# Performance work log

Hardware: AMD Instinct MI355X
Metric: run time of the kernel (lower is better)

Reference implementation:

```python
import jax, jax.numpy as jnp
import numpy as np

DIM = 192
HEADS = 6
HEAD_DIM = DIM // HEADS
WS = (7, 7, 7)
SHIFT = (3, 3, 3)
RES = (14, 56, 56)
MLP_HIDDEN = DIM * 4
N = WS[0] * WS[1] * WS[2]  # 343 tokens per window
SCALE = HEAD_DIM ** (-0.5)


def _rel_pos_index():
    coords = np.stack(np.meshgrid(np.arange(WS[0]), np.arange(WS[1]), np.arange(WS[2]), indexing='ij'))
    cf = coords.reshape(3, -1)  # (3, N)
    rel = (cf[:, :, None] - cf[:, None, :]).transpose(1, 2, 0).astype(np.int64)  # (N, N, 3)
    rel[..., 0] += WS[0] - 1
    rel[..., 1] += WS[1] - 1
    rel[..., 2] += WS[2] - 1
    rel[..., 0] *= (2 * WS[1] - 1) * (2 * WS[2] - 1)
    rel[..., 1] *= 2 * WS[2] - 1
    return rel.sum(-1)  # (N, N)


def _attn_mask():
    S, H, W = RES
    img = np.zeros((S, H, W), dtype=np.float32)
    cnt = 0
    for s in (slice(0, -WS[0]), slice(-WS[0], -SHIFT[0]), slice(-SHIFT[0], None)):
        for h in (slice(0, -WS[1]), slice(-WS[1], -SHIFT[1]), slice(-SHIFT[1], None)):
            for w in (slice(0, -WS[2]), slice(-WS[2], -SHIFT[2]), slice(-SHIFT[2], None)):
                img[s, h, w] = cnt
                cnt += 1
    m = img.reshape(S // WS[0], WS[0], H // WS[1], WS[1], W // WS[2], WS[2])
    m = m.transpose(0, 2, 4, 1, 3, 5).reshape(-1, N)  # (nW, N)
    diff = m[:, None, :] - m[:, :, None]
    return np.where(diff != 0, -100.0, 0.0).astype(np.float32)  # (nW, N, N)


REL_IDX = jnp.asarray(_rel_pos_index())
ATTN_MASK = jnp.asarray(_attn_mask())


def _window_partition(x):
    # x: (B, S, H, W, C) -> (B*nW, N, C)
    B, S, H, W, C = x.shape
    x = x.reshape(B, S // WS[0], WS[0], H // WS[1], WS[1], W // WS[2], WS[2], C)
    x = x.transpose(0, 1, 3, 5, 2, 4, 6, 7)
    return x.reshape(-1, N, C)


def _window_reverse(wins, B):
    S, H, W = RES
    C = wins.shape[-1]
    x = wins.reshape(B, S // WS[0], H // WS[1], W // WS[2], WS[0], WS[1], WS[2], C)
    x = x.transpose(0, 1, 4, 2, 5, 3, 6, 7)
    return x.reshape(B, S, H, W, C)


def _layernorm(x, g, b):
    mu = x.mean(-1, keepdims=True)
    var = ((x - mu) ** 2).mean(-1, keepdims=True)
    return (x - mu) * jax.lax.rsqrt(var + 1e-5) * g + b


def setup_inputs() -> dict:
    key = jax.random.key(0)
    ks = jax.random.split(key, 16)
    p = lambda k, shape, s=0.02: (jax.random.normal(k, shape, dtype=jnp.float32) * s)
    return {
        'x': jax.random.normal(ks[0], (1, DIM) + RES, dtype=jnp.float32),
        'norm1_g': jnp.ones((DIM,), jnp.float32),
        'norm1_b': jnp.zeros((DIM,), jnp.float32),
        'qkv_w': p(ks[1], (DIM, 3 * DIM)),
        'qkv_b': jnp.zeros((3 * DIM,), jnp.float32),
        'rpb_table': p(ks[2], ((2 * WS[0] - 1) * (2 * WS[1] - 1) * (2 * WS[2] - 1), HEADS)),
        'proj_w': p(ks[3], (DIM, DIM)),
        'proj_b': jnp.zeros((DIM,), jnp.float32),
        'norm2_g': jnp.ones((DIM,), jnp.float32),
        'norm2_b': jnp.zeros((DIM,), jnp.float32),
        'fc1_w': p(ks[4], (DIM, MLP_HIDDEN)),
        'fc1_b': jnp.zeros((MLP_HIDDEN,), jnp.float32),
        'fc2_w': p(ks[5], (MLP_HIDDEN, DIM)),
        'fc2_b': jnp.zeros((DIM,), jnp.float32),
    }


def reference(x, norm1_g, norm1_b, qkv_w, qkv_b, rpb_table, proj_w, proj_b,
              norm2_g, norm2_b, fc1_w, fc1_b, fc2_w, fc2_b):
    B, C, S, H, W = x.shape
    L = S * H * W
    xt = x.transpose(0, 2, 3, 4, 1).reshape(B, L, C)  # b (s h w) c
    shortcut = xt
    xn = _layernorm(xt, norm1_g, norm1_b).reshape(B, S, H, W, C)
    xs = jnp.roll(xn, (-SHIFT[0], -SHIFT[1], -SHIFT[2]), axis=(1, 2, 3))
    xw = _window_partition(xs)  # (B*nW, N, C)
    B_ = xw.shape[0]
    nW = B_ // B

    qkv = (xw @ qkv_w + qkv_b).reshape(B_, N, 3, HEADS, HEAD_DIM)
    q = qkv[:, :, 0].transpose(0, 2, 1, 3) * SCALE  # (B_, h, N, d)
    k = qkv[:, :, 1].transpose(0, 2, 1, 3)
    v = qkv[:, :, 2].transpose(0, 2, 1, 3)

    attn = jnp.einsum('bhnd,bhmd->bhnm', q, k)
    bias = rpb_table[REL_IDX.reshape(-1)].reshape(N, N, HEADS).transpose(2, 0, 1)  # (h, N, N)
    attn = attn + bias[None]
    attn = attn.reshape(B, nW, HEADS, N, N) + ATTN_MASK[None, :, None]
    attn = jax.nn.softmax(attn.reshape(B_, HEADS, N, N), axis=-1)

    out = jnp.einsum('bhnm,bhmd->bhnd', attn, v).transpose(0, 2, 1, 3).reshape(B_, N, C)
    out = out @ proj_w + proj_b

    xr = _window_reverse(out, B)
    xr = jnp.roll(xr, (SHIFT[0], SHIFT[1], SHIFT[2]), axis=(1, 2, 3)).reshape(B, L, C)
    xt = shortcut + xr

    h = _layernorm(xt, norm2_g, norm2_b)
    h = jax.nn.gelu(h @ fc1_w + fc1_b, approximate=False) @ fc2_w + fc2_b
    xt = xt + h

    return xt.reshape(B, S, H, W, C).transpose(0, 4, 1, 2, 3)  # (B, C, S, H, W)
```

## Files before the change

### kernel.cpp

```cpp
#include <hip/hip_runtime.h>
#include <hip/hip_bf16.h>
#include <math.h>

#define L_TOK 43904
#define NWIN 128
#define NTOK 343
#define NHEAD 6
#define SCALE 0.17677669529663687f
#define LOG2E 1.4426950408889634f
#define NMASK -144.26950408889634f
#define BSTRIDE 352
#define FIXMAX 16.0f

typedef __attribute__((ext_vector_type(8))) short short8;
typedef __attribute__((ext_vector_type(4))) float f32x4;

__device__ __forceinline__ unsigned short f2bf(float x) {
    union { float f; unsigned int u; } v; v.f = x;
    unsigned int r = v.u + 0x7fffu + ((v.u >> 16) & 1u);
    return (unsigned short)(r >> 16);
}
__device__ __forceinline__ unsigned int cvtpk(float a, float b) {
    unsigned int r;
    asm volatile("v_cvt_pk_bf16_f32 %0, %1, %2" : "=v"(r) : "v"(a), "v"(b));
    return r;
}
__device__ __forceinline__ void gload16(const void* g, void* l) {
    __builtin_amdgcn_global_load_lds((const __attribute__((address_space(1))) void*)g,
                                     (__attribute__((address_space(3))) void*)l, 16, 0, 0);
}

__device__ __forceinline__ int winrow(int l) {
    int s = l / 3136;
    int rem = l - s * 3136;
    int h = rem / 56;
    int w = rem - h * 56;
    int ps = s + 11; if (ps >= 14) ps -= 14;
    int ph = h + 53; if (ph >= 56) ph -= 56;
    int pw = w + 53; if (pw >= 56) pw -= 56;
    int wi = ((ps / 7) * 8 + ph / 7) * 8 + pw / 7;
    int tk = ((ps % 7) * 7 + ph % 7) * 7 + pw % 7;
    return wi * NTOK + tk;
}

__global__ __launch_bounds__(256) void prep_kernel(
    const float* __restrict__ qkv_w, const float* __restrict__ qkv_b,
    const float* __restrict__ proj_w, const float* __restrict__ fc1_w,
    const float* __restrict__ fc2_w, const float* __restrict__ table,
    unsigned short* __restrict__ qkvT, unsigned short* __restrict__ projT,
    unsigned short* __restrict__ fc1T, unsigned short* __restrict__ fc2T,
    float* __restrict__ qkvb_s, float* __restrict__ biasC) {
    const float qs = SCALE * LOG2E;
    if (blockIdx.x < 576) {
        int stride = 576 * 256;
        int t0 = blockIdx.x * 256 + threadIdx.x;
        for (int i = t0; i < 576 * 192; i += stride) {
            int n = i / 192, k = i - n * 192;
            float v = qkv_w[k * 576 + n];
            if (n < 192) v *= qs;
            qkvT[i] = f2bf(v);
        }
        for (int i = t0; i < 192 * 192; i += stride) {
            int n = i / 192, k = i - n * 192;
            projT[i] = f2bf(proj_w[k * 192 + n]);
        }
        for (int i = t0; i < 768 * 192; i += stride) {
            int n = i / 192, k = i - n * 192;
            fc1T[i] = f2bf(fc1_w[k * 768 + n]);
        }
        for (int i = t0; i < 192 * 768; i += stride) {
            int n = i / 768, k = i - n * 768;
            fc2T[i] = f2bf(fc2_w[k * 192 + n]);
        }
        for (int i = t0; i < 576; i += stride) {
            float v = qkv_b[i]; if (i < 192) v *= qs;
            qkvb_s[i] = v;
        }
    } else {
        int q = blockIdx.x - 576;
        int qs3 = q / 49, qh = (q / 7) % 7, qw = q % 7;
        for (int k = threadIdx.x; k < BSTRIDE; k += 256) {
            if (k < NTOK) {
                int ks = k / 49, kh = (k / 7) % 7, kw = k % 7;
                int idx = ((qs3 - ks + 6) * 13 + (qh - kh + 6)) * 13 + (qw - kw + 6);
                #pragma unroll
                for (int h = 0; h < NHEAD; ++h)
                    biasC[((size_t)h * NTOK + q) * BSTRIDE + k] = table[idx * 6 + h] * LOG2E - FIXMAX;
            } else {
                #pragma unroll
                for (int h = 0; h < NHEAD; ++h)
                    biasC[((size_t)h * NTOK + q) * BSTRIDE + k] = -30000.f;
            }
        }
    }
}

__global__ __launch_bounds__(256) void ln1_part(const float* __restrict__ x,
                                                const float* __restrict__ g, const float* __restrict__ b,
                                                float* __restrict__ xt, unsigned short* __restrict__ xw) {
    __shared__ float tile[192 * 65];
    __shared__ float red[4][64];
    __shared__ float red2[4][64];
    __shared__ float mu_s[64], rs_s[64];
    int l0 = blockIdx.x * 64;
    int tid = threadIdx.x;
    int j = tid & 63, c4 = tid >> 6;
    for (int cb = 0; cb < 192; cb += 4)
        tile[(cb + c4) * 65 + j] = x[(size_t)(cb + c4) * L_TOK + l0 + j];
    __syncthreads();
    float s = 0.f, ss = 0.f;
    for (int c = c4 * 48; c < c4 * 48 + 48; ++c) {
        float v = tile[c * 65 + j];
        s += v; ss += v * v;
    }
    red[c4][j] = s; red2[c4][j] = ss;
    __syncthreads();
    if (tid < 64) {
        float S = red[0][j] + red[1][j] + red[2][j] + red[3][j];
        float SS = red2[0][j] + red2[1][j] + red2[2][j] + red2[3][j];
        float mu = S * (1.f / 192.f);
        float var = SS * (1.f / 192.f) - mu * mu;
        mu_s[j] = mu;
        rs_s[j] = rsqrtf(var + 1e-5f);
    }
    __syncthreads();
    int wave = tid >> 6, lid = tid & 63;
    for (int t = wave; t < 64; t += 4) {
        int l = l0 + t;
        int r = winrow(l);
        float mu = mu_s[t], rs = rs_s[t];
        #pragma unroll
        for (int q = 0; q < 3; ++q) {
            int c = q * 64 + lid;
            float v = tile[c * 65 + t];
            xt[(size_t)l * 192 + c] = v;
            xw[(size_t)r * 192 + c] = f2bf((v - mu) * rs * g[c] + b[c]);
        }
    }
}

template<int EPI, int OUTMODE>
__global__ __launch_bounds__(256, 3) void gemm_bf16(
    const unsigned short* __restrict__ A, const unsigned short* __restrict__ Bt,
    const float* __restrict__ bias, void* __restrict__ Cout,
    const float* __restrict__ xt, int N, int K) {
    __shared__ unsigned char smem[49152];
    unsigned short* sh = (unsigned short*)smem;
    const int tid = threadIdx.x;
    const int m0 = blockIdx.y * 128;
    const int n0 = blockIdx.x * 64;
    const int lane = tid & 63, wv = tid >> 6;
    const int wm = wv >> 1, wn = wv & 1;
    const int lr = lane & 15, lg = lane >> 4;
    const int KT = K >> 6;

    f32x4 acc[4][2];
    #pragma unroll
    for (int i = 0; i < 4; ++i)
        #pragma unroll
        for (int jj = 0; jj < 2; ++jj)
            acc[i][jj] = (f32x4){0.f, 0.f, 0.f, 0.f};

    #define STAGE(BUF, K0) { \
        unsigned short* dst = sh + (BUF) * 12288; \
        _Pragma("unroll") \
        for (int i_ = 0; i_ < 4; ++i_) { \
            int g_ = (i_ * 4 + wv) * 64 + lane; \
            int row_ = g_ >> 3, gc_ = g_ & 7; \
            gload16(A + (size_t)(m0 + row_) * K + (K0) + ((gc_ ^ (row_ & 7)) << 3), dst + g_ * 8); \
        } \
        _Pragma("unroll") \
        for (int i_ = 0; i_ < 2; ++i_) { \
            int g_ = (i_ * 4 + wv) * 64 + lane; \
            int row_ = g_ >> 3, gc_ = g_ & 7; \
            gload16(Bt + (size_t)(n0 + row_) * K + (K0) + ((gc_ ^ (row_ & 7)) << 3), dst + 8192 + g_ * 8); \
        } }

    STAGE(0, 0);
    __syncthreads();
    for (int kt = 0; kt < KT; ++kt) {
        int buf = kt & 1;
        if (kt + 1 < KT) STAGE(buf ^ 1, (kt + 1) << 6);
        const unsigned short* sA = sh + buf * 12288;
        const unsigned short* sB = sA + 8192;
        #pragma unroll
        for (int kk = 0; kk < 2; ++kk) {
            short8 a[4], b[2];
            #pragma unroll
            for (int i = 0; i < 4; ++i) {
                int row = wm * 64 + i * 16 + lr;
                a[i] = *(const short8*)(sA + row * 64 + (((kk * 4 + lg) ^ (lr & 7)) << 3));
            }
            #pragma unroll
            for (int jj = 0; jj < 2; ++jj) {
                int row = wn * 32 + jj * 16 + lr;
                b[jj] = *(const short8*)(sB + row * 64 + (((kk * 4 + lg) ^ (lr & 7)) << 3));
            }
            #pragma unroll
            for (int i = 0; i < 4; ++i)
                #pragma unroll
                for (int jj = 0; jj < 2; ++jj)
                    acc[i][jj] = __builtin_amdgcn_mfma_f32_16x16x32_bf16(a[i], b[jj], acc[i][jj], 0, 0, 0);
        }
        __syncthreads();
    }
    #undef STAGE

    if (OUTMODE == 2) {
        float* Cs = (float*)smem;
        #pragma unroll
        for (int i = 0; i < 4; ++i)
            #pragma unroll
            for (int jj = 0; jj < 2; ++jj)
                #pragma unroll
                for (int r = 0; r < 4; ++r) {
                    int row = wm * 64 + i * 16 + lg * 4 + r;
                    int col = wn * 32 + jj * 16 + lr;
                    float v = acc[i][jj][r] + bias[n0 + col] + xt[(size_t)(m0 + row) * 192 + n0 + col];
                    Cs[row * 68 + col] = v;
                }
        __syncthreads();
        float* outp = (float*)Cout;
        int c = tid & 63;
        #pragma unroll
        for (int j4 = tid >> 6; j4 < 32; j4 += 4) {
            f32x4 v;
            #pragma unroll
            for (int t = 0; t < 4; ++t) v[t] = Cs[(j4 * 4 + t) * 68 + c];
            *(f32x4*)&outp[(size_t)(n0 + c) * L_TOK + m0 + j4 * 4] = v;
        }
    } else {
        float bia[2];
        bia[0] = bias[n0 + wn * 32 + lr];
        bia[1] = bias[n0 + wn * 32 + 16 + lr];
        #pragma unroll
        for (int i = 0; i < 4; ++i) {
            #pragma unroll
            for (int jj = 0; jj < 2; ++jj) {
                #pragma unroll
                for (int r = 0; r < 4; ++r) {
                    float v = acc[i][jj][r] + bia[jj];
                    if (EPI == 1) v = 0.5f * v * (1.f + erff(v * 0.70710678118654752f));
                    int row = m0 + wm * 64 + i * 16 + lg * 4 + r;
                    int col = n0 + wn * 32 + jj * 16 + lr;
                    if (OUTMODE == 1) ((float*)Cout)[(size_t)row * N + col] = v;
                    else ((unsigned short*)Cout)[(size_t)row * N + col] = f2bf(v);
                }
            }
        }
    }
}

__global__ __launch_bounds__(256) void gemm_proj_ln(
    const unsigned short* __restrict__ A, const unsigned short* __restrict__ Bt,
    const float* __restrict__ bias, const float* __restrict__ g2, const float* __restrict__ b2,
    float* __restrict__ xt, unsigned short* __restrict__ h1) {
    __shared__ unsigned short As[2][64 * 64];
    __shared__ unsigned short Bs[2][192 * 64];
    const int tid = threadIdx.x;
    const int m0 = blockIdx.x * 64;
    const int lane = tid & 63, wv = tid >> 6;
    const int lr = lane & 15, lg = lane >> 4;
    const int K = 192;

    f32x4 acc[12];
    #pragma unroll
    for (int jj = 0; jj < 12; ++jj) acc[jj] = (f32x4){0.f, 0.f, 0.f, 0.f};

    #define PSTAGE(BUF, K0) { \
        _Pragma("unroll") \
        for (int i_ = 0; i_ < 2; ++i_) { \
            int g_ = i_ * 256 + tid; \
            int row_ = g_ >> 3, gc_ = g_ & 7; \
            gload16(A + (size_t)(m0 + row_) * K + (K0) + ((gc_ ^ (row_ & 7)) << 3), &As[BUF][g_ * 8]); \
        } \
        _Pragma("unroll") \
        for (int i_ = 0; i_ < 6; ++i_) { \
            int g_ = i_ * 256 + tid; \
            int row_ = g_ >> 3, gc_ = g_ & 7; \
            gload16(Bt + (size_t)row_ * K + (K0) + ((gc_ ^ (row_ & 7)) << 3), &Bs[BUF][g_ * 8]); \
        } }

    PSTAGE(0, 0);
    __syncthreads();
    for (int kt = 0; kt < 3; ++kt) {
        int buf = kt & 1;
        if (kt + 1 < 3) PSTAGE(buf ^ 1, (kt + 1) << 6);
        #pragma unroll
        for (int kk = 0; kk < 2; ++kk) {
            int arow = wv * 16 + lr;
            short8 a = *(const short8*)(&As[buf][arow * 64 + (((kk * 4 + lg) ^ (lr & 7)) << 3)]);
            #pragma unroll
            for (int jj = 0; jj < 12; ++jj) {
                int brow = jj * 16 + lr;
                short8 b = *(const short8*)(&Bs[buf][brow * 64 + (((kk * 4 + lg) ^ (lr & 7)) << 3)]);
                acc[jj] = __builtin_amdgcn_mfma_f32_16x16x32_bf16(a, b, acc[jj], 0, 0, 0);
            }
        }
        __syncthreads();
    }
    #undef PSTAGE

    #pragma unroll
    for (int r = 0; r < 4; ++r) {
        int m = m0 + wv * 16 + lg * 4 + r;
        int wi = m / 343, tk = m - wi * 343;
        int ts = tk / 49, rm = tk - ts * 49, th = rm / 7, tw = rm - th * 7;
        int ps = (wi >> 6) * 7 + ts, ph = ((wi >> 3) & 7) * 7 + th, pw = (wi & 7) * 7 + tw;
        int ss_ = ps + 3; if (ss_ >= 14) ss_ -= 14;
        int hh = ph + 3; if (hh >= 56) hh -= 56;
        int ww = pw + 3; if (ww >= 56) ww -= 56;
        size_t l = ((size_t)ss_ * 56 + hh) * 56 + ww;
        float val[12];
        float sum = 0.f, ssum = 0.f;
        #pragma unroll
        for (int jj = 0; jj < 12; ++jj) {
            int col = jj * 16 + lr;
            float v = acc[jj][r] + bias[col] + xt[l * 192 + col];
            xt[l * 192 + col] = v;
            val[jj] = v; sum += v; ssum += v * v;
        }
        #pragma unroll
        for (int off = 1; off < 16; off <<= 1) {
            sum += __shfl_xor(sum, off);
            ssum += __shfl_xor(ssum, off);
        }
        float mu = sum * (1.f / 192.f);
        float rs = rsqrtf(ssum * (1.f / 192.f) - mu * mu + 1e-5f);
        #pragma unroll
        for (int jj = 0; jj < 12; ++jj) {
            int col = jj * 16 + lr;
            h1[l * 192 + col] = f2bf((val[jj] - mu) * rs * g2[col] + b2[col]);
        }
    }
}

__global__ __launch_bounds__(256) void attn_flash(
    const unsigned short* __restrict__ qkv, const float* __restrict__ biasC,
    unsigned short* __restrict__ aout) {
    __shared__ unsigned short Ks[352 * 32];
    __shared__ unsigned short Vt[32][360];
    __shared__ unsigned int Ps2[4][16][20];
    __shared__ unsigned char regq[352];
    const int w = blockIdx.x, h = blockIdx.y;
    const int tid = threadIdx.x;
    const size_t base = (size_t)w * NTOK * 576;
    const bool interior = ((w >> 6) == 0) && (((w >> 3) & 7) != 7) && ((w & 7) != 7);

    for (int g = tid; g < 1372; g += 256) {
        int row = g >> 2, c = g & 3;
        gload16(qkv + base + (size_t)row * 576 + 192 + h * 32 + ((c ^ ((row >> 1) & 3)) << 3), Ks + g * 8);
    }
    if (tid < 36) {
        short8 z = {};
        *(short8*)(Ks + (343 + (tid >> 2)) * 32 + (tid & 3) * 8) = z;
    }
    for (int idx = tid; idx < 688; idx += 256) {
        int jp = idx >> 2, c = idx & 3;
        int j0 = jp * 2, j1 = j0 + 1;
        short8 v0 = *(const short8*)(qkv + base + (size_t)j0 * 576 + 384 + h * 32 + c * 8);
        short8 v1 = {};
        if (j1 < NTOK) v1 = *(const short8*)(qkv + base + (size_t)j1 * 576 + 384 + h * 32 + c * 8);
        #pragma unroll
        for (int i = 0; i < 8; ++i) {
            ushort2 pr; pr.x = (unsigned short)v0[i]; pr.y = (unsigned short)v1[i];
            *(ushort2*)&Vt[c * 8 + i][j0] = pr;
        }
    }
    for (int idx = tid; idx < 128; idx += 256) {
        ushort2 z; z.x = 0; z.y = 0;
        *(ushort2*)&Vt[idx >> 2][344 + (idx & 3) * 2] = z;
    }
    if (!interior) {
        const int wis = w >> 6, wih = (w >> 3) & 7, wiw = w & 7;
        for (int n = tid; n < 352; n += 256) {
            unsigned char rv = 0;
            if (n < NTOK) {
                int ts = n / 49, r49 = n - ts * 49, th = r49 / 7, tw = r49 - th * 7;
                int ps = wis * 7 + ts, ph = wih * 7 + th, pw = wiw * 7 + tw;
                int rs = ps < 7 ? 0 : (ps < 11 ? 1 : 2);
                int rh = ph < 49 ? 0 : (ph < 53 ? 1 : 2);
                int rw = pw < 49 ? 0 : (pw < 53 ? 1 : 2);
                rv = (unsigned char)(rs * 9 + rh * 3 + rw);
            }
            regq[n] = rv;
        }
    }
    __syncthreads();

    const int wid = tid >> 6, l = tid & 63, lr = l & 15, lg = l >> 4;
    const int kchunk = (lg ^ ((lr >> 1) & 3)) << 3;

    for (int qt = wid; qt < 22; qt += 4) {
        int qrow = qt * 16 + lr;
        int qr = qrow < NTOK ? qrow : NTOK - 1;
        short8 qa = *(const short8*)(qkv + base + (size_t)qr * 576 + h * 32 + lg * 8);
        const float* bq = biasC + ((size_t)h * NTOK + qr) * BSTRIDE + lg * 4;

        float lsum = 0.f;
        f32x4 o0 = (f32x4){0.f, 0.f, 0.f, 0.f};
        f32x4 o1 = (f32x4){0.f, 0.f, 0.f, 0.f};
        const f32x4 zv = (f32x4){0.f, 0.f, 0.f, 0.f};

        if (interior) {
            #pragma unroll 2
            for (int kb = 0; kb < 11; ++kb) {
                const int kt0 = 2 * kb, kt1 = 2 * kb + 1;
                short8 k0 = *(const short8*)(Ks + (kt0 * 16 + lr) * 32 + kchunk);
                short8 k1 = *(const short8*)(Ks + (kt1 * 16 + lr) * 32 + kchunk);
                __builtin_amdgcn_s_setprio(1);
                f32x4 s0 = __builtin_amdgcn_mfma_f32_16x16x32_bf16(k0, qa, zv, 0, 0, 0);
                f32x4 s1 = __builtin_amdgcn_mfma_f32_16x16x32_bf16(k1, qa, zv, 0, 0, 0);
                __builtin_amdgcn_s_setprio(0);
                f32x4 bv0 = *(const f32x4*)(bq + kt0 * 16);
                f32x4 bv1 = *(const f32x4*)(bq + kt1 * 16);
                f32x4 p0, p1;
                #pragma unroll
                for (int r = 0; r < 4; ++r) {
                    p0[r] = exp2f(s0[r] + bv0[r]);
                    p1[r] = exp2f(s1[r] + bv1[r]);
                    lsum += p0[r] + p1[r];
                }
                Ps2[wid][lr][lg * 2 + 0] = cvtpk(p0[0], p0[1]);
                Ps2[wid][lr][lg * 2 + 1] = cvtpk(p0[2], p0[3]);
                Ps2[wid][lr][8 + lg * 2 + 0] = cvtpk(p1[0], p1[1]);
                Ps2[wid][lr][8 + lg * 2 + 1] = cvtpk(p1[2], p1[3]);
                short8 pa = *(const short8*)&Ps2[wid][lr][lg * 4];
                short8 v0 = *(const short8*)&Vt[lr][kb * 32 + lg * 8];
                short8 v1 = *(const short8*)&Vt[16 + lr][kb * 32 + lg * 8];
                __builtin_amdgcn_s_setprio(1);
                o0 = __builtin_amdgcn_mfma_f32_16x16x32_bf16(pa, v0, o0, 0, 0, 0);
                o1 = __builtin_amdgcn_mfma_f32_16x16x32_bf16(pa, v1, o1, 0, 0, 0);
                __builtin_amdgcn_s_setprio(0);
            }
        } else {
            unsigned int rq = regq[qr];
            #pragma unroll 2
            for (int kb = 0; kb < 11; ++kb) {
                const int kt0 = 2 * kb, kt1 = 2 * kb + 1;
                short8 k0 = *(const short8*)(Ks + (kt0 * 16 + lr) * 32 + kchunk);
                short8 k1 = *(const short8*)(Ks + (kt1 * 16 + lr) * 32 + kchunk);
                __builtin_amdgcn_s_setprio(1);
                f32x4 s0 = __builtin_amdgcn_mfma_f32_16x16x32_bf16(k0, qa, zv, 0, 0, 0);
                f32x4 s1 = __builtin_amdgcn_mfma_f32_16x16x32_bf16(k1, qa, zv, 0, 0, 0);
                __builtin_amdgcn_s_setprio(0);
                f32x4 bv0 = *(const f32x4*)(bq + kt0 * 16);
                f32x4 bv1 = *(const f32x4*)(bq + kt1 * 16);
                unsigned int rb0 = *(const unsigned int*)&regq[kt0 * 16 + lg * 4];
                unsigned int rb1 = *(const unsigned int*)&regq[kt1 * 16 + lg * 4];
                f32x4 p0, p1;
                #pragma unroll
                for (int r = 0; r < 4; ++r) {
                    float m0 = (((rb0 >> (r * 8)) & 255u) != rq) ? NMASK : 0.f;
                    float m1 = (((rb1 >> (r * 8)) & 255u) != rq) ? NMASK : 0.f;
                    p0[r] = exp2f(s0[r] + bv0[r] + m0);
                    p1[r] = exp2f(s1[r] + bv1[r] + m1);
                    lsum += p0[r] + p1[r];
                }
                Ps2[wid][lr][lg * 2 + 0] = cvtpk(p0[0], p0[1]);
                Ps2[wid][lr][lg * 2 + 1] = cvtpk(p0[2], p0[3]);
                Ps2[wid][lr][8 + lg * 2 + 0] = cvtpk(p1[0], p1[1]);
                Ps2[wid][lr][8 + lg * 2 + 1] = cvtpk(p1[2], p1[3]);
                short8 pa = *(const short8*)&Ps2[wid][lr][lg * 4];
                short8 v0 = *(const short8*)&Vt[lr][kb * 32 + lg * 8];
                short8 v1 = *(const short8*)&Vt[16 + lr][kb * 32 + lg * 8];
                __builtin_amdgcn_s_setprio(1);
                o0 = __builtin_amdgcn_mfma_f32_16x16x32_bf16(pa, v0, o0, 0, 0, 0);
                o1 = __builtin_amdgcn_mfma_f32_16x16x32_bf16(pa, v1, o1, 0, 0, 0);
                __builtin_amdgcn_s_setprio(0);
            }
        }
        lsum += __shfl_xor(lsum, 16);
        lsum += __shfl_xor(lsum, 32);
        float inv = 1.f / lsum;

        #pragma unroll
        for (int r = 0; r < 4; ++r) {
            float iv = __shfl(inv, lg * 4 + r);
            int q = qt * 16 + lg * 4 + r;
            if (q < NTOK) {
                size_t orow = ((size_t)w * NTOK + q) * 192 + h * 32;
                aout[orow + lr] = f2bf(o0[r] * iv);
                aout[orow + 16 + lr] = f2bf(o1[r] * iv);
            }
        }
    }
}

extern "C" void kernel_launch(void* const* d_in, const int* in_sizes, int n_in,
                              void* d_out, int out_size, void* d_ws, size_t ws_size,
                              hipStream_t stream) {
    const float* x      = (const float*)d_in[0];
    const float* n1g    = (const float*)d_in[1];
    const float* n1b    = (const float*)d_in[2];
    const float* qkv_w  = (const float*)d_in[3];
    const float* qkv_b  = (const float*)d_in[4];
    const float* rpb    = (const float*)d_in[5];
    const float* proj_w = (const float*)d_in[6];
    const float* proj_b = (const float*)d_in[7];
    const float* n2g    = (const float*)d_in[8];
    const float* n2b    = (const float*)d_in[9];
    const float* fc1_w  = (const float*)d_in[10];
    const float* fc1_b  = (const float*)d_in[11];
    const float* fc2_w  = (const float*)d_in[12];
    const float* fc2_b  = (const float*)d_in[13];
    float* out = (float*)d_out;

    char* p = (char*)d_ws;
    float* xt = (float*)p;                     p += (size_t)L_TOK * 192 * 4;
    unsigned short* xw = (unsigned short*)p;
    unsigned short* h1 = xw;                   p += (size_t)L_TOK * 192 * 2;
    unsigned short* qkvb = (unsigned short*)p;
    unsigned short* h2 = qkvb;                 p += (size_t)L_TOK * 768 * 2;
    unsigned short* aoutb = (unsigned short*)p; p += (size_t)L_TOK * 192 * 2;
    float* biasC = (float*)p;                  p += (size_t)NHEAD * NTOK * BSTRIDE * 4 + 256;
    unsigned short* qkvT = (unsigned short*)p; p += (size_t)576 * 192 * 2;
    unsigned short* projT = (unsigned short*)p; p += (size_t)192 * 192 * 2;
    unsigned short* fc1T = (unsigned short*)p; p += (size_t)768 * 192 * 2;
    unsigned short* fc2T = (unsigned short*)p; p += (size_t)192 * 768 * 2;
    float* qkvb_s = (float*)p;                 p += 576 * 4;

    prep_kernel<<<919, 256, 0, stream>>>(qkv_w, qkv_b, proj_w, fc1_w, fc2_w, rpb,
                                         qkvT, projT, fc1T, fc2T, qkvb_s, biasC);
    ln1_part<<<686, 256, 0, stream>>>(x, n1g, n1b, xt, xw);
    gemm_bf16<0, 0><<<dim3(9, 343), 256, 0, stream>>>(xw, qkvT, qkvb_s, qkvb, nullptr, 576, 192);
    attn_flash<<<dim3(NWIN, NHEAD), 256, 0, stream>>>(qkvb, biasC, aoutb);
    gemm_proj_ln<<<686, 256, 0, stream>>>(aoutb, projT, proj_b, n2g, n2b, xt, h1);
    gemm_bf16<1, 0><<<dim3(12, 343), 256, 0, stream>>>(h1, fc1T, fc1_b, h2, nullptr, 768, 192);
    gemm_bf16<0, 2><<<dim3(3, 343), 256, 0, stream>>>(h2, fc2T, fc2_b, out, xt, 192, 768);
}
```

Baseline: 221.6 us.

## Add K=192 GEMM kernel keeping A row-tile in LDS, streaming B from global

Replaces the generic tiled GEMM for the QKV and FC1 projections with a specialised kernel. Each block loads a 64x192 A tile into swizzled LDS once, then loops over all output columns, reading B fragments directly from global memory (weights are small and L2-resident) with no LDS staging or per-tile barriers. This is meant to remove repeated A reloads across column blocks and the synchronisation overhead of the generic kernel. In exchange it has less parallelism per block (686 blocks doing long serial loops), only 16 rows per wave, and uncoalesced scalar bf16 stores and uncached global B reads.

```diff
diff --git a/kernel.cpp b/kernel.cpp
--- a/kernel.cpp
+++ b/kernel.cpp
@@ -139,10 +139,60 @@
     }
 }
 
-template<int EPI, int OUTMODE>
-__global__ __launch_bounds__(256, 3) void gemm_bf16(
+template<int EPI>
+__global__ __launch_bounds__(256) void gemm_k192(
     const unsigned short* __restrict__ A, const unsigned short* __restrict__ Bt,
-    const float* __restrict__ bias, void* __restrict__ Cout,
+    const float* __restrict__ bias, unsigned short* __restrict__ Cout, int N) {
+    __shared__ unsigned short As[64 * 192];
+    const int tid = threadIdx.x;
+    const int m0 = blockIdx.x * 64;
+    const int lane = tid & 63, wv = tid >> 6;
+    const int lr = lane & 15, lg = lane >> 4;
+
+    #pragma unroll
+    for (int i = 0; i < 6; ++i) {
+        int g = i * 256 + tid;
+        int row = g / 24, gc = g - row * 24;
+        gload16(A + (size_t)(m0 + row) * 192 + ((gc ^ (row & 7)) << 3), As + g * 8);
+    }
+    __syncthreads();
+
+    const unsigned short* Arow = As + (wv * 16 + lr) * 192;
+    const int asw = lr & 7;
+
+    const int NT = N >> 5;
+    #pragma unroll 1
+    for (int nt = 0; nt < NT; ++nt) {
+        const int n0 = nt * 32;
+        f32x4 acc[2];
+        acc[0] = (f32x4){0.f, 0.f, 0.f, 0.f};
+        acc[1] = (f32x4){0.f, 0.f, 0.f, 0.f};
+        #pragma unroll
+        for (int kt = 0; kt < 6; ++kt) {
+            short8 a = *(const short8*)(Arow + (((kt * 4 + lg) ^ asw) << 3));
+            #pragma unroll
+            for (int jj = 0; jj < 2; ++jj) {
+                short8 b = *(const short8*)(Bt + (size_t)(n0 + jj * 16 + lr) * 192 + kt * 32 + lg * 8);
+                acc[jj] = __builtin_amdgcn_mfma_f32_16x16x32_bf16(a, b, acc[jj], 0, 0, 0);
+            }
+        }
+        #pragma unroll
+        for (int jj = 0; jj < 2; ++jj) {
+            float bb = bias[n0 + jj * 16 + lr];
+            #pragma unroll
+            for (int r = 0; r < 4; ++r) {
+                float v = acc[jj][r] + bb;
+                if (EPI == 1) v = 0.5f * v * (1.f + erff(v * 0.70710678118654752f));
+                int row = m0 + wv * 16 + lg * 4 + r;
+                Cout[(size_t)row * N + n0 + jj * 16 + lr] = f2bf(v);
+            }
+        }
+    }
+}
+
+__global__ __launch_bounds__(256, 3) void gemm_fc2(
+    const unsigned short* __restrict__ A, const unsigned short* __restrict__ Bt,
+    const float* __restrict__ bias, float* __restrict__ outp,
     const float* __restrict__ xt, int N, int K) {
     __shared__ unsigned char smem[49152];
     unsigned short* sh = (unsigned short*)smem;
@@ -206,48 +256,26 @@
     }
     #undef STAGE
 
-    if (OUTMODE == 2) {
-        float* Cs = (float*)smem;
-        #pragma unroll
-        for (int i = 0; i < 4; ++i)
-            #pragma unroll
-            for (int jj = 0; jj < 2; ++jj)
-                #pragma unroll
-                for (int r = 0; r < 4; ++r) {
-                    int row = wm * 64 + i * 16 + lg * 4 + r;
-                    int col = wn * 32 + jj * 16 + lr;
-                    float v = acc[i][jj][r] + bias[n0 + col] + xt[(size_t)(m0 + row) * 192 + n0 + col];
-                    Cs[row * 68 + col] = v;
-                }
-        __syncthreads();
-        float* outp = (float*)Cout;
-        int c = tid & 63;
-        #pragma unroll
-        for (int j4 = tid >> 6; j4 < 32; j4 += 4) {
-            f32x4 v;
-            #pragma unroll
-            for (int t = 0; t < 4; ++t) v[t] = Cs[(j4 * 4 + t) * 68 + c];
-            *(f32x4*)&outp[(size_t)(n0 + c) * L_TOK + m0 + j4 * 4] = v;
-        }
-    } else {
-        float bia[2];
-        bia[0] = bias[n0 + wn * 32 + lr];
-        bia[1] = bias[n0 + wn * 32 + 16 + lr];
-        #pragma unroll
-        for (int i = 0; i < 4; ++i) {
-            #pragma unroll
-            for (int jj = 0; jj < 2; ++jj) {
-                #pragma unroll
-                for (int r = 0; r < 4; ++r) {
-                    float v = acc[i][jj][r] + bia[jj];
-                    if (EPI == 1) v = 0.5f * v * (1.f + erff(v * 0.70710678118654752f));
-                    int row = m0 + wm * 64 + i * 16 + lg * 4 + r;
-                    int col = n0 + wn * 32 + jj * 16 + lr;
-                    if (OUTMODE == 1) ((float*)Cout)[(size_t)row * N + col] = v;
-                    else ((unsigned short*)Cout)[(size_t)row * N + col] = f2bf(v);
-                }
-            }
-        }
+    float* Cs = (float*)smem;
+    #pragma unroll
+    for (int i = 0; i < 4; ++i)
+        #pragma unroll
+        for (int jj = 0; jj < 2; ++jj)
+            #pragma unroll
+            for (int r = 0; r < 4; ++r) {
+                int row = wm * 64 + i * 16 + lg * 4 + r;
+                int col = wn * 32 + jj * 16 + lr;
+                float v = acc[i][jj][r] + bias[n0 + col] + xt[(size_t)(m0 + row) * 192 + n0 + col];
+                Cs[row * 68 + col] = v;
+            }
+    __syncthreads();
+    int c = tid & 63;
+    #pragma unroll
+    for (int j4 = tid >> 6; j4 < 32; j4 += 4) {
+        f32x4 v;
+        #pragma unroll
+        for (int t = 0; t < 4; ++t) v[t] = Cs[(j4 * 4 + t) * 68 + c];
+        *(f32x4*)&outp[(size_t)(n0 + c) * L_TOK + m0 + j4 * 4] = v;
     }
 }
 
@@ -523,9 +551,9 @@
     prep_kernel<<<919, 256, 0, stream>>>(qkv_w, qkv_b, proj_w, fc1_w, fc2_w, rpb,
                                          qkvT, projT, fc1T, fc2T, qkvb_s, biasC);
     ln1_part<<<686, 256, 0, stream>>>(x, n1g, n1b, xt, xw);
-    gemm_bf16<0, 0><<<dim3(9, 343), 256, 0, stream>>>(xw, qkvT, qkvb_s, qkvb, nullptr, 576, 192);
+    gemm_k192<0><<<686, 256, 0, stream>>>(xw, qkvT, qkvb_s, qkvb, 576);
     attn_flash<<<dim3(NWIN, NHEAD), 256, 0, stream>>>(qkvb, biasC, aoutb);
     gemm_proj_ln<<<686, 256, 0, stream>>>(aoutb, projT, proj_b, n2g, n2b, xt, h1);
-    gemm_bf16<1, 0><<<dim3(12, 343), 256, 0, stream>>>(h1, fc1T, fc1_b, h2, nullptr, 768, 192);
-    gemm_bf16<0, 2><<<dim3(3, 343), 256, 0, stream>>>(h2, fc2T, fc2_b, out, xt, 192, 768);
-}
+    gemm_k192<1><<<686, 256, 0, stream>>>(h1, fc1T, fc1_b, h2, 768);
+    gemm_fc2<<<dim3(3, 343), 256, 0, stream>>>(h2, fc2T, fc2_b, out, xt, 192, 768);
+}
```

After: 334.3 us. 1.51x slower.
